# Kernel optimization log

Measured on AMD Instinct MI355X. Metric: run time of the kernel, lower is better.

The kernel has to match this reference:

```python
import jax, jax.numpy as jnp
import numpy as np

LAM = 0.3          # margin weight lam (halved inside, as in the torch code)
IGNORE = 255       # ignore_index
NEG = -1e30        # finite -inf stand-in for masking the label class


def setup_inputs() -> dict:
    key = jax.random.key(0)
    k1, k2 = jax.random.split(key)
    logits = jax.random.normal(k1, (8, 19, 512, 512), dtype=jnp.float32)
    labels = jax.random.randint(k2, (8, 512, 512), 0, 19)  # no ignored pixels
    return {"logits": logits, "labels": labels}


def _loss_per_pixel(logits, lb):
    # logits: (N, C, H, W) float32, lb: (N, H, W) int in [0, C)
    C = logits.shape[1]
    coeff = 1.0 / (C - 1.0)
    lam = LAM / 2.0
    onehot = jax.nn.one_hot(lb, C, axis=1, dtype=jnp.bool_)  # (N, C, H, W)
    # softmax over the C-1 non-label classes == softmax with label class masked out
    m_logits = jnp.where(onehot, NEG, logits)
    log_q = jax.nn.log_softmax(m_logits, axis=1)
    q = jnp.exp(log_q)
    margin = jnp.where(onehot, 0.0, (q - coeff) * log_q).sum(axis=1) * lam  # (N, H, W)
    # standard cross-entropy term: -log_softmax(logits)[label]
    log_p = jax.nn.log_softmax(logits, axis=1)
    ce = -jnp.take_along_axis(log_p, lb[:, None], axis=1)[:, 0]  # (N, H, W)
    return margin + ce


def reference(logits, labels):
    valid = labels != IGNORE
    lb = jnp.where(valid, labels, 0)
    loss = _loss_per_pixel(logits.astype(jnp.float32), lb)
    vf = valid.astype(loss.dtype)
    # reduction='mean' over non-ignored pixels
    return (loss * vf).sum() / vf.sum()
```

## Files before the change

kernel.cpp:

```cpp
#include <hip/hip_runtime.h>

#define NCLS 19
#define HW (512 * 512)
#define NPIX (8 * HW)
#define TILE 512
#define NBLK (NPIX / TILE)
#define NTHR 512
#define CHUNKS (NCLS * TILE / 4)

__global__ __launch_bounds__(NTHR, 8) void lms_main_kernel(
    const float* __restrict__ logits, const int* __restrict__ labels,
    float* __restrict__ partials) {
  const float COEFF = 1.0f / 18.0f;
  const float LAM_HALF = 0.15f;

  __shared__ float tile[NCLS * TILE];

  const int t = threadIdx.x;
  const long pixel0 = (long)blockIdx.x * TILE;
  const int n = blockIdx.x >> 9;
  const int hw0 = (blockIdx.x & 511) * TILE;
  const float* gbase = logits + (size_t)n * NCLS * HW + hw0;

#pragma unroll
  for (int f = t; f < CHUNKS; f += NTHR) {
    int r = f >> 7;
    int col = f & 127;
    const float* g = gbase + (size_t)r * HW + col * 4;
    const __attribute__((address_space(1))) float* g1 =
        (const __attribute__((address_space(1))) float*)(uintptr_t)g;
    __attribute__((address_space(3))) float* l3 =
        (__attribute__((address_space(3))) float*)(uintptr_t)(&tile[f * 4]);
    __builtin_amdgcn_global_load_lds(g1, l3, 16, 0, 0);
  }

  int lb = labels[pixel0 + t];
  int l = (lb != 255) ? lb : 0;

  __syncthreads();

  float s = 0.f, T = 0.f, S = 0.f;
#pragma unroll
  for (int c = 0; c < NCLS; ++c) {
    float v = tile[c * TILE + t];
    float e = __expf(v);
    s += e;
    T += e * v;
    S += v;
  }
  float xl = tile[l * TILE + t];

  float el = __expf(xl);
  float sm = s - el;
  float margin = (T - el * xl) / sm - COEFF * (S - xl);
  float ce = __logf(s) - xl;
  bool valid = (lb != 255);
  float loss = valid ? (ce + LAM_HALF * margin) : 0.f;
  float cnt = valid ? 1.f : 0.f;

#pragma unroll
  for (int off = 32; off > 0; off >>= 1) {
    loss += __shfl_down(loss, off, 64);
    cnt += __shfl_down(cnt, off, 64);
  }
  __shared__ float sl[8], sc[8];
  int wave = t >> 6;
  int lane = t & 63;
  if (lane == 0) {
    sl[wave] = loss;
    sc[wave] = cnt;
  }
  __syncthreads();
  if (t == 0) {
    float L = 0.f, C = 0.f;
#pragma unroll
    for (int w = 0; w < 8; ++w) {
      L += sl[w];
      C += sc[w];
    }
    partials[2 * blockIdx.x] = L;
    partials[2 * blockIdx.x + 1] = C;
  }
}

__global__ __launch_bounds__(1024) void lms_final_kernel(
    const float* __restrict__ partials, float* __restrict__ out) {
  int t = threadIdx.x;
  float loss = 0.f, cnt = 0.f;
#pragma unroll
  for (int k = 0; k < 4; ++k) {
    float2 pr = ((const float2*)partials)[t + 1024 * k];
    loss += pr.x;
    cnt += pr.y;
  }
#pragma unroll
  for (int off = 32; off > 0; off >>= 1) {
    loss += __shfl_down(loss, off, 64);
    cnt += __shfl_down(cnt, off, 64);
  }
  __shared__ float sl[16], sc[16];
  int wave = t >> 6;
  int lane = t & 63;
  if (lane == 0) {
    sl[wave] = loss;
    sc[wave] = cnt;
  }
  __syncthreads();
  if (t == 0) {
    float L = 0.f, C = 0.f;
#pragma unroll
    for (int w = 0; w < 16; ++w) {
      L += sl[w];
      C += sc[w];
    }
    out[0] = L / C;
  }
}

extern "C" void kernel_launch(void* const* d_in, const int* in_sizes, int n_in,
                              void* d_out, int out_size, void* d_ws, size_t ws_size,
                              hipStream_t stream) {
  const float* logits = (const float*)d_in[0];
  const int* labels = (const int*)d_in[1];
  float* out = (float*)d_out;
  float* partials = (float*)d_ws;

  lms_main_kernel<<<NBLK, NTHR, 0, stream>>>(logits, labels, partials);
  lms_final_kernel<<<1, 1024, 0, stream>>>(partials, out);
}
```

Before: 223.7 us.

## Fuse final reduction via last-block atomic counter and rotate class load order

Result: slower. 423.5 us (+89.3%).

```diff
diff --git a/kernel.cpp b/kernel.cpp
--- a/kernel.cpp
+++ b/kernel.cpp
@@ -8,9 +8,12 @@
 #define NTHR 512
 #define CHUNKS (NCLS * TILE / 4)
 
+#define CTR_OFF 32768
+
 __global__ __launch_bounds__(NTHR, 8) void lms_main_kernel(
     const float* __restrict__ logits, const int* __restrict__ labels,
-    float* __restrict__ partials) {
+    float* __restrict__ partials, unsigned int* __restrict__ counter,
+    float* __restrict__ out) {
   const float COEFF = 1.0f / 18.0f;
   const float LAM_HALF = 0.15f;
 
@@ -21,16 +24,19 @@
   const int n = blockIdx.x >> 9;
   const int hw0 = (blockIdx.x & 511) * TILE;
   const float* gbase = logits + (size_t)n * NCLS * HW + hw0;
+  const int rot = blockIdx.x % NCLS;
 
 #pragma unroll
   for (int f = t; f < CHUNKS; f += NTHR) {
-    int r = f >> 7;
+    int fr = f >> 7;
     int col = f & 127;
+    int r = fr + rot;
+    if (r >= NCLS) r -= NCLS;
     const float* g = gbase + (size_t)r * HW + col * 4;
     const __attribute__((address_space(1))) float* g1 =
         (const __attribute__((address_space(1))) float*)(uintptr_t)g;
     __attribute__((address_space(3))) float* l3 =
-        (__attribute__((address_space(3))) float*)(uintptr_t)(&tile[f * 4]);
+        (__attribute__((address_space(3))) float*)(uintptr_t)(&tile[r * TILE + col * 4]);
     __builtin_amdgcn_global_load_lds(g1, l3, 16, 0, 0);
   }
 
@@ -64,6 +70,7 @@
     cnt += __shfl_down(cnt, off, 64);
   }
   __shared__ float sl[8], sc[8];
+  __shared__ int lastFlag;
   int wave = t >> 6;
   int lane = t & 63;
   if (lane == 0) {
@@ -80,40 +87,40 @@
     }
     partials[2 * blockIdx.x] = L;
     partials[2 * blockIdx.x + 1] = C;
-  }
-}
-
-__global__ __launch_bounds__(1024) void lms_final_kernel(
-    const float* __restrict__ partials, float* __restrict__ out) {
-  int t = threadIdx.x;
-  float loss = 0.f, cnt = 0.f;
-#pragma unroll
-  for (int k = 0; k < 4; ++k) {
-    float2 pr = ((const float2*)partials)[t + 1024 * k];
-    loss += pr.x;
-    cnt += pr.y;
-  }
-#pragma unroll
-  for (int off = 32; off > 0; off >>= 1) {
-    loss += __shfl_down(loss, off, 64);
-    cnt += __shfl_down(cnt, off, 64);
-  }
-  __shared__ float sl[16], sc[16];
-  int wave = t >> 6;
-  int lane = t & 63;
-  if (lane == 0) {
-    sl[wave] = loss;
-    sc[wave] = cnt;
+    __threadfence();
+    unsigned int old = atomicAdd(counter, 1u);
+    lastFlag = (old == NBLK - 1);
   }
   __syncthreads();
-  if (t == 0) {
+
+  if (lastFlag) {
+    __threadfence();
     float L = 0.f, C = 0.f;
 #pragma unroll
-    for (int w = 0; w < 16; ++w) {
-      L += sl[w];
-      C += sc[w];
+    for (int k = 0; k < NBLK / NTHR; ++k) {
+      float2 pr = ((const float2*)partials)[t + NTHR * k];
+      L += pr.x;
+      C += pr.y;
     }
-    out[0] = L / C;
+#pragma unroll
+    for (int off = 32; off > 0; off >>= 1) {
+      L += __shfl_down(L, off, 64);
+      C += __shfl_down(C, off, 64);
+    }
+    if (lane == 0) {
+      sl[wave] = L;
+      sc[wave] = C;
+    }
+    __syncthreads();
+    if (t == 0) {
+      float Lt = 0.f, Ct = 0.f;
+#pragma unroll
+      for (int w = 0; w < 8; ++w) {
+        Lt += sl[w];
+        Ct += sc[w];
+      }
+      out[0] = Lt / Ct;
+    }
   }
 }
 
@@ -124,7 +131,9 @@
   const int* labels = (const int*)d_in[1];
   float* out = (float*)d_out;
   float* partials = (float*)d_ws;
+  unsigned int* counter = (unsigned int*)((char*)d_ws + CTR_OFF);
 
-  lms_main_kernel<<<NBLK, NTHR, 0, stream>>>(logits, labels, partials);
-  lms_final_kernel<<<1, 1024, 0, stream>>>(partials, out);
+  hipMemsetAsync(counter, 0, sizeof(unsigned int), stream);
+  lms_main_kernel<<<NBLK, NTHR, 0, stream>>>(logits, labels, partials, counter,
+                                             out);
 }
```
